# Optimization experiments

Hardware: AMD Instinct MI355X
Metric: run time of the kernel (lower is better)

The kernel has to match this reference:

```python
import jax, jax.numpy as jnp
import numpy as np

TEMPERATURE = 0.5


def setup_inputs() -> dict:
    key = jax.random.key(0)
    k1, k2 = jax.random.split(key)
    B, D = 4096, 256
    emb_i = jax.random.normal(k1, (B, D), dtype=jnp.float32)
    emb_j = jax.random.normal(k2, (B, D), dtype=jnp.float32)
    return {"emb_i": emb_i, "emb_j": emb_j}


def reference(emb_i, emb_j):
    B = emb_i.shape[0]
    # L2-normalize along feature dim (torch F.normalize uses eps=1e-12 clamp)
    def l2norm(x):
        n = jnp.sqrt(jnp.sum(x * x, axis=1, keepdims=True))
        return x / jnp.maximum(n, 1e-12)

    z_i = l2norm(emb_i)
    z_j = l2norm(emb_j)
    reps = jnp.concatenate([z_i, z_j], axis=0)  # [2B, D]
    # cosine similarity of normalized rows == plain GEMM
    sim = (reps @ reps.T) / TEMPERATURE  # [2B, 2B]
    # mask out self-similarity on the diagonal
    diag = jnp.eye(2 * B, dtype=bool)
    sim = jnp.where(diag, -jnp.inf, sim)
    # labels: row i -> i+B, row B+i -> i
    labels = jnp.concatenate([jnp.arange(B) + B, jnp.arange(B)])
    logp = jax.nn.log_softmax(sim, axis=1)
    loss = -jnp.mean(jnp.take_along_axis(logp, labels[:, None], axis=1))
    return loss
```

## Files before the change

### kernel.cpp

```cpp
#include <hip/hip_runtime.h>

typedef __bf16 bf16x8 __attribute__((ext_vector_type(8)));
typedef float f32x4 __attribute__((ext_vector_type(4)));

#define D_DIM 256
#define C2 2.88539008f
#define LN2 0.69314718f

__device__ __forceinline__ unsigned short f2bf(float f) {
  union { float f; unsigned u; } x; x.f = f;
  unsigned r = x.u + 0x7FFFu + ((x.u >> 16) & 1u);
  return (unsigned short)(r >> 16);
}

__global__ __launch_bounds__(256) void k_normalize(const float* __restrict__ ei,
                                                   const float* __restrict__ ej,
                                                   unsigned short* __restrict__ R,
                                                   unsigned* __restrict__ ticket,
                                                   int B) {
  if (blockIdx.x == 0 && threadIdx.x == 0) *ticket = 0u;
  const int w = threadIdx.x >> 6, lane = threadIdx.x & 63;
  const int row = blockIdx.x * 4 + w;
  const float* src = (row < B) ? (ei + (size_t)row * D_DIM)
                               : (ej + (size_t)(row - B) * D_DIM);
  float4 v = reinterpret_cast<const float4*>(src)[lane];
  float ss = v.x * v.x + v.y * v.y + v.z * v.z + v.w * v.w;
#pragma unroll
  for (int d = 32; d; d >>= 1) ss += __shfl_xor(ss, d, 64);
  float s = 1.0f / fmaxf(sqrtf(ss), 1e-12f);
  ushort4 o;
  o.x = f2bf(v.x * s); o.y = f2bf(v.y * s);
  o.z = f2bf(v.z * s); o.w = f2bf(v.w * s);
  reinterpret_cast<ushort4*>(R + (size_t)row * D_DIM)[lane] = o;
}

__global__ __launch_bounds__(256, 4) void k_simgemm(const unsigned short* __restrict__ R,
                                                    float* __restrict__ rowPartial,
                                                    float* __restrict__ simTgt,
                                                    int N) {
  __shared__ char lds[2][16 * 1024];
  const int tid = threadIdx.x;
  const int w = tid >> 6, lane = tid & 63;
  const int wr = w >> 1, wc = w & 1;
  const int half = N >> 1;

  const int T = N / 128;
  const int t = blockIdx.x;
  int bi = (int)(((float)(2 * T + 1) -
                  sqrtf((float)((2 * T + 1) * (2 * T + 1) - 8 * t))) * 0.5f);
  while (bi > 0 && t < bi * (2 * T - bi + 1) / 2) --bi;
  while (t >= (bi + 1) * (2 * T - bi) / 2) ++bi;
  const int bj = bi + (t - bi * (2 * T - bi + 1) / 2);
  const int brow = bi * 128, bcol = bj * 128;
  const bool offdiag = (bi != bj);

  f32x4 zero4 = {0.f, 0.f, 0.f, 0.f};
  f32x4 acc[4][4];
#pragma unroll
  for (int m = 0; m < 4; ++m)
#pragma unroll
    for (int n = 0; n < 4; ++n) acc[m][n] = zero4;

  auto stage = [&](int buf, int kt) {
    char* dst = lds[buf];
#pragma unroll
    for (int i = 0; i < 4; ++i) {
      const int grp = i * 4 + w;
      const int cp = (grp & 7) * 64 + lane;
      const int r = cp >> 2, js = cp & 3;
      const int j = js ^ ((r >> 1) & 3);
      const int base = (grp < 8) ? brow : bcol;
      const unsigned short* g = R + (size_t)(base + r) * D_DIM + kt * 32 + j * 8;
      __builtin_amdgcn_global_load_lds(
          (const __attribute__((address_space(1))) void*)g,
          (__attribute__((address_space(3))) void*)(dst + (size_t)grp * 1024), 16, 0, 0);
    }
  };

  auto compute = [&](int buf) {
    const char* ldsA = lds[buf];
    const char* ldsB = lds[buf] + 8 * 1024;
    const int k8 = lane >> 4;
    bf16x8 a[4], b[4];
#pragma unroll
    for (int m = 0; m < 4; ++m) {
      const int row = wr * 64 + m * 16 + (lane & 15);
      a[m] = *reinterpret_cast<const bf16x8*>(ldsA + (row * 4 + (k8 ^ ((row >> 1) & 3))) * 16);
    }
#pragma unroll
    for (int n = 0; n < 4; ++n) {
      const int col = wc * 64 + n * 16 + (lane & 15);
      b[n] = *reinterpret_cast<const bf16x8*>(ldsB + (col * 4 + (k8 ^ ((col >> 1) & 3))) * 16);
    }
#pragma unroll
    for (int m = 0; m < 4; ++m)
#pragma unroll
      for (int n = 0; n < 4; ++n)
        acc[m][n] = __builtin_amdgcn_mfma_f32_16x16x32_bf16(a[m], b[n], acc[m][n], 0, 0, 0);
  };

  stage(0, 0);
#pragma unroll
  for (int kt = 0; kt < 8; ++kt) {
    const int cur = kt & 1;
    if (kt < 7) {
      stage(cur ^ 1, kt + 1);
      asm volatile("s_waitcnt vmcnt(4)" ::: "memory");
    } else {
      asm volatile("s_waitcnt vmcnt(0)" ::: "memory");
    }
    __builtin_amdgcn_s_barrier();
    compute(cur);
    __builtin_amdgcn_s_barrier();
  }

  float cs[4] = {0.f, 0.f, 0.f, 0.f};
#pragma unroll
  for (int m = 0; m < 4; ++m) {
#pragma unroll
    for (int j = 0; j < 4; ++j) {
      const int gr = brow + wr * 64 + m * 16 + (lane >> 4) * 4 + j;
      const int tgt = (gr < half) ? gr + half : gr - half;
      float rs = 0.f;
#pragma unroll
      for (int n = 0; n < 4; ++n) {
        const int gc = bcol + wc * 64 + n * 16 + (lane & 15);
        const float sv2 = acc[m][n][j] * C2;
        const float ev = (gr == gc) ? 0.f : __builtin_amdgcn_exp2f(sv2);
        if (gc == tgt) {
          simTgt[gr] = sv2;
          if (offdiag) simTgt[gc] = sv2;
        }
        rs += ev;
        cs[n] += ev;
      }
#pragma unroll
      for (int d = 1; d < 16; d <<= 1) rs += __shfl_xor(rs, d, 64);
      if ((lane & 15) == 0)
        rowPartial[(size_t)(bj * 2 + wc) * N + gr] = rs;
    }
  }
  if (offdiag) {
#pragma unroll
    for (int n = 0; n < 4; ++n) {
      float c = cs[n];
      c += __shfl_xor(c, 16, 64);
      c += __shfl_xor(c, 32, 64);
      if ((lane >> 4) == 0)
        rowPartial[(size_t)(bi * 2 + wr) * N + (bcol + wc * 64 + n * 16 + lane)] = c;
    }
  }
}

__global__ __launch_bounds__(256) void k_rowreduce(const float* __restrict__ rowPartial,
                                                   const float* __restrict__ simTgt,
                                                   float* __restrict__ blockOut,
                                                   unsigned* __restrict__ ticket,
                                                   float* __restrict__ out, int N) {
  const int row = blockIdx.x * 256 + threadIdx.x;
  float denom = 0.f;
#pragma unroll 8
  for (int c = 0; c < 128; ++c) denom += rowPartial[(size_t)c * N + row];
  float lossr = (__builtin_amdgcn_logf(denom) - simTgt[row]) * LN2;
#pragma unroll
  for (int d = 32; d; d >>= 1) lossr += __shfl_xor(lossr, d, 64);
  __shared__ float red[4];
  __shared__ int isLast;
  if ((threadIdx.x & 63) == 0) red[threadIdx.x >> 6] = lossr;
  __syncthreads();
  if (threadIdx.x == 0) {
    atomicExch(&blockOut[blockIdx.x], red[0] + red[1] + red[2] + red[3]);
    isLast = (atomicAdd(ticket, 1u) == gridDim.x - 1);
  }
  __syncthreads();
  if (isLast && threadIdx.x < 64) {
    float v = (threadIdx.x < gridDim.x) ? atomicAdd(&blockOut[threadIdx.x], 0.0f) : 0.f;
#pragma unroll
    for (int d = 32; d; d >>= 1) v += __shfl_xor(v, d, 64);
    if (threadIdx.x == 0) out[0] = v / (float)N;
  }
}

extern "C" void kernel_launch(void* const* d_in, const int* in_sizes, int n_in,
                              void* d_out, int out_size, void* d_ws, size_t ws_size,
                              hipStream_t stream) {
  const float* ei = (const float*)d_in[0];
  const float* ej = (const float*)d_in[1];
  const int B = in_sizes[0] / D_DIM;
  const int N = 2 * B;

  char* ws = (char*)d_ws;
  unsigned short* R = (unsigned short*)ws;
  float* rowPartial = (float*)(ws + (size_t)N * D_DIM * 2);
  float* simTgt     = (float*)(ws + (size_t)N * D_DIM * 2 + (size_t)128 * N * 4);
  float* blockOut   = (float*)((char*)simTgt + (size_t)N * 4);
  unsigned* ticket  = (unsigned*)((char*)blockOut + (size_t)(N / 256) * 4);

  k_normalize<<<N / 4, 256, 0, stream>>>(ei, ej, R, ticket, B);
  const int T = N / 128;
  k_simgemm<<<T * (T + 1) / 2, 256, 0, stream>>>(R, rowPartial, simTgt, N);
  k_rowreduce<<<N / 256, 256, 0, stream>>>(rowPartial, simTgt, blockOut, ticket,
                                           (float*)d_out, N);
}
```

Measured before the change: 49.09 us.

## Load GEMM operands directly from global into registers, dropping LDS staging

The similarity GEMM no longer stages A/B tiles through double-buffered shared memory with global_load_lds and barriers. Each wave now loads its MFMA fragments straight from global memory (relying on L1/L2 caching) and drops the occupancy hint from launch_bounds. This removes the LDS round trip and the block barriers, but each tile is now fetched redundantly by two waves, the loads are 16-byte gathers across rows, and without prefetch or software pipelining the global load latency is exposed before each MFMA group.

```diff
diff --git a/kernel.cpp b/kernel.cpp
--- a/kernel.cpp
+++ b/kernel.cpp
@@ -34,11 +34,10 @@
   reinterpret_cast<ushort4*>(R + (size_t)row * D_DIM)[lane] = o;
 }
 
-__global__ __launch_bounds__(256, 4) void k_simgemm(const unsigned short* __restrict__ R,
-                                                    float* __restrict__ rowPartial,
-                                                    float* __restrict__ simTgt,
-                                                    int N) {
-  __shared__ char lds[2][16 * 1024];
+__global__ __launch_bounds__(256) void k_simgemm(const unsigned short* __restrict__ R,
+                                                 float* __restrict__ rowPartial,
+                                                 float* __restrict__ simTgt,
+                                                 int N) {
   const int tid = threadIdx.x;
   const int w = tid >> 6, lane = tid & 63;
   const int wr = w >> 1, wc = w & 1;
@@ -61,57 +60,23 @@
 #pragma unroll
     for (int n = 0; n < 4; ++n) acc[m][n] = zero4;
 
-  auto stage = [&](int buf, int kt) {
-    char* dst = lds[buf];
+  const unsigned short* aBase = R + (size_t)(brow + wr * 64 + (lane & 15)) * D_DIM + (lane >> 4) * 8;
+  const unsigned short* bBase = R + (size_t)(bcol + wc * 64 + (lane & 15)) * D_DIM + (lane >> 4) * 8;
+
 #pragma unroll
-    for (int i = 0; i < 4; ++i) {
-      const int grp = i * 4 + w;
-      const int cp = (grp & 7) * 64 + lane;
-      const int r = cp >> 2, js = cp & 3;
-      const int j = js ^ ((r >> 1) & 3);
-      const int base = (grp < 8) ? brow : bcol;
-      const unsigned short* g = R + (size_t)(base + r) * D_DIM + kt * 32 + j * 8;
-      __builtin_amdgcn_global_load_lds(
-          (const __attribute__((address_space(1))) void*)g,
-          (__attribute__((address_space(3))) void*)(dst + (size_t)grp * 1024), 16, 0, 0);
-    }
-  };
-
-  auto compute = [&](int buf) {
-    const char* ldsA = lds[buf];
-    const char* ldsB = lds[buf] + 8 * 1024;
-    const int k8 = lane >> 4;
+  for (int kt = 0; kt < 8; ++kt) {
     bf16x8 a[4], b[4];
 #pragma unroll
-    for (int m = 0; m < 4; ++m) {
-      const int row = wr * 64 + m * 16 + (lane & 15);
-      a[m] = *reinterpret_cast<const bf16x8*>(ldsA + (row * 4 + (k8 ^ ((row >> 1) & 3))) * 16);
-    }
+    for (int m = 0; m < 4; ++m)
+      a[m] = *reinterpret_cast<const bf16x8*>(aBase + (size_t)m * 16 * D_DIM + kt * 32);
 #pragma unroll
-    for (int n = 0; n < 4; ++n) {
-      const int col = wc * 64 + n * 16 + (lane & 15);
-      b[n] = *reinterpret_cast<const bf16x8*>(ldsB + (col * 4 + (k8 ^ ((col >> 1) & 3))) * 16);
-    }
+    for (int n = 0; n < 4; ++n)
+      b[n] = *reinterpret_cast<const bf16x8*>(bBase + (size_t)n * 16 * D_DIM + kt * 32);
 #pragma unroll
     for (int m = 0; m < 4; ++m)
 #pragma unroll
       for (int n = 0; n < 4; ++n)
         acc[m][n] = __builtin_amdgcn_mfma_f32_16x16x32_bf16(a[m], b[n], acc[m][n], 0, 0, 0);
-  };
-
-  stage(0, 0);
-#pragma unroll
-  for (int kt = 0; kt < 8; ++kt) {
-    const int cur = kt & 1;
-    if (kt < 7) {
-      stage(cur ^ 1, kt + 1);
-      asm volatile("s_waitcnt vmcnt(4)" ::: "memory");
-    } else {
-      asm volatile("s_waitcnt vmcnt(0)" ::: "memory");
-    }
-    __builtin_amdgcn_s_barrier();
-    compute(cur);
-    __builtin_amdgcn_s_barrier();
   }
 
   float cs[4] = {0.f, 0.f, 0.f, 0.f};
```

Result: slower. 95.20 us (+93.9%).

## Triple-buffer GEMM LDS pipeline and split row reduction across warps

Applied to the files above, without the earlier changes.

The similarity GEMM now keeps three LDS stages instead of two, so loads for two K-steps ahead are in flight while the current stage is computed. This is meant to hide global-load latency, at the cost of more shared memory and a lower occupancy hint (3 blocks per CU). The row-reduce kernel now splits each row's 128 partial sums across four warps, combines them through shared memory and launches four times as many blocks. That raises memory-level parallelism for the strided partial reads. The final combine reads 128 per-block values and relies on there being exactly 128 reduce blocks.

```diff
diff --git a/kernel.cpp b/kernel.cpp
--- a/kernel.cpp
+++ b/kernel.cpp
@@ -34,11 +34,11 @@
   reinterpret_cast<ushort4*>(R + (size_t)row * D_DIM)[lane] = o;
 }
 
-__global__ __launch_bounds__(256, 4) void k_simgemm(const unsigned short* __restrict__ R,
+__global__ __launch_bounds__(256, 3) void k_simgemm(const unsigned short* __restrict__ R,
                                                     float* __restrict__ rowPartial,
                                                     float* __restrict__ simTgt,
                                                     int N) {
-  __shared__ char lds[2][16 * 1024];
+  __shared__ char lds[3][16 * 1024];
   const int tid = threadIdx.x;
   const int w = tid >> 6, lane = tid & 63;
   const int wr = w >> 1, wc = w & 1;
@@ -100,17 +100,19 @@
   };
 
   stage(0, 0);
+  stage(1, 1);
 #pragma unroll
   for (int kt = 0; kt < 8; ++kt) {
-    const int cur = kt & 1;
-    if (kt < 7) {
-      stage(cur ^ 1, kt + 1);
+    if (kt < 6) {
+      stage((kt + 2) % 3, kt + 2);
+      asm volatile("s_waitcnt vmcnt(8)" ::: "memory");
+    } else if (kt == 6) {
       asm volatile("s_waitcnt vmcnt(4)" ::: "memory");
     } else {
       asm volatile("s_waitcnt vmcnt(0)" ::: "memory");
     }
     __builtin_amdgcn_s_barrier();
-    compute(cur);
+    compute(kt % 3);
     __builtin_amdgcn_s_barrier();
   }
 
@@ -157,24 +159,31 @@
                                                    float* __restrict__ blockOut,
                                                    unsigned* __restrict__ ticket,
                                                    float* __restrict__ out, int N) {
-  const int row = blockIdx.x * 256 + threadIdx.x;
-  float denom = 0.f;
+  const int lane = threadIdx.x & 63;
+  const int q = threadIdx.x >> 6;
+  const int row = blockIdx.x * 64 + lane;
+  float part = 0.f;
 #pragma unroll 8
-  for (int c = 0; c < 128; ++c) denom += rowPartial[(size_t)c * N + row];
-  float lossr = (__builtin_amdgcn_logf(denom) - simTgt[row]) * LN2;
-#pragma unroll
-  for (int d = 32; d; d >>= 1) lossr += __shfl_xor(lossr, d, 64);
-  __shared__ float red[4];
+  for (int c = q * 32; c < q * 32 + 32; ++c)
+    part += rowPartial[(size_t)c * N + row];
+  __shared__ float red[4][64];
   __shared__ int isLast;
-  if ((threadIdx.x & 63) == 0) red[threadIdx.x >> 6] = lossr;
+  red[q][lane] = part;
   __syncthreads();
-  if (threadIdx.x == 0) {
-    atomicExch(&blockOut[blockIdx.x], red[0] + red[1] + red[2] + red[3]);
-    isLast = (atomicAdd(ticket, 1u) == gridDim.x - 1);
+  if (threadIdx.x < 64) {
+    const float denom = red[0][lane] + red[1][lane] + red[2][lane] + red[3][lane];
+    float lossr = (__builtin_amdgcn_logf(denom) - simTgt[row]) * LN2;
+#pragma unroll
+    for (int d = 32; d; d >>= 1) lossr += __shfl_xor(lossr, d, 64);
+    if (threadIdx.x == 0) {
+      atomicExch(&blockOut[blockIdx.x], lossr);
+      isLast = (atomicAdd(ticket, 1u) == gridDim.x - 1);
+    }
   }
   __syncthreads();
   if (isLast && threadIdx.x < 64) {
-    float v = (threadIdx.x < gridDim.x) ? atomicAdd(&blockOut[threadIdx.x], 0.0f) : 0.f;
+    float v = atomicAdd(&blockOut[threadIdx.x], 0.0f) +
+              atomicAdd(&blockOut[64 + threadIdx.x], 0.0f);
 #pragma unroll
     for (int d = 32; d; d >>= 1) v += __shfl_xor(v, d, 64);
     if (threadIdx.x == 0) out[0] = v / (float)N;
@@ -194,11 +203,11 @@
   float* rowPartial = (float*)(ws + (size_t)N * D_DIM * 2);
   float* simTgt     = (float*)(ws + (size_t)N * D_DIM * 2 + (size_t)128 * N * 4);
   float* blockOut   = (float*)((char*)simTgt + (size_t)N * 4);
-  unsigned* ticket  = (unsigned*)((char*)blockOut + (size_t)(N / 256) * 4);
+  unsigned* ticket  = (unsigned*)((char*)blockOut + 128 * 4);
 
   k_normalize<<<N / 4, 256, 0, stream>>>(ei, ej, R, ticket, B);
   const int T = N / 128;
   k_simgemm<<<T * (T + 1) / 2, 256, 0, stream>>>(R, rowPartial, simTgt, N);
-  k_rowreduce<<<N / 256, 256, 0, stream>>>(rowPartial, simTgt, blockOut, ticket,
-                                           (float*)d_out, N);
-}
+  k_rowreduce<<<N / 64, 256, 0, stream>>>(rowPartial, simTgt, blockOut, ticket,
+                                          (float*)d_out, N);
+}
```

New measurement: 49.41 us. About the same (+0.7%).
